# Kernel optimization log

Measured on AMD Instinct MI355X. Metric: run time of the kernel, lower is better.

Reference implementation:

```python
import jax, jax.numpy as jnp
import numpy as np

N = 100_000   # num nodes
E = 3_200_000 # num directed edges (before self-loops)
NEG_SLOPE = 0.2


def setup_inputs() -> dict:
    key = jax.random.key(0)
    ks = jax.random.split(key, 12)
    x = jax.random.normal(ks[0], (N, 2), jnp.float32)
    edge_index = jax.random.randint(ks[1], (2, E), 0, N, dtype=jnp.int32)
    # GATConv(2, 16): lin weight [2,16] (no bias), att_src/att_dst [16], out bias [16]
    W1 = jax.random.normal(ks[2], (2, 16), jnp.float32) * (1.0 / np.sqrt(2.0))
    a_src1 = jax.random.normal(ks[3], (16,), jnp.float32) * 0.25
    a_dst1 = jax.random.normal(ks[4], (16,), jnp.float32) * 0.25
    b1 = jnp.zeros((16,), jnp.float32)
    # GATConv(16, 64)
    W2 = jax.random.normal(ks[5], (16, 64), jnp.float32) * (1.0 / np.sqrt(16.0))
    a_src2 = jax.random.normal(ks[6], (64,), jnp.float32) * 0.125
    a_dst2 = jax.random.normal(ks[7], (64,), jnp.float32) * 0.125
    b2 = jnp.zeros((64,), jnp.float32)
    return {"x": x, "edge_index": edge_index,
            "W1": W1, "a_src1": a_src1, "a_dst1": a_dst1, "b1": b1,
            "W2": W2, "a_src2": a_src2, "a_dst2": a_dst2, "b2": b2}


def _gat_layer(x, src, dst, W, a_src, a_dst, b):
    # x: [N, Fin]; src/dst: [E'] (self-loops included). Single head, PyG GATConv math.
    h = x @ W                                        # [N, Fout]
    alpha_s = h @ a_src                              # [N]
    alpha_d = h @ a_dst                              # [N]
    e = jax.nn.leaky_relu(alpha_s[src] + alpha_d[dst], NEG_SLOPE)  # [E']
    # segment softmax over incoming edges of each dst node
    m = jax.ops.segment_max(e, dst, num_segments=N)
    m = jnp.where(jnp.isfinite(m), m, 0.0)           # nodes always have a self-loop, but be safe
    p = jnp.exp(e - m[dst])
    s = jax.ops.segment_sum(p, dst, num_segments=N)
    alpha = p / s[dst]                               # [E']
    out = jax.ops.segment_sum(alpha[:, None] * h[src], dst, num_segments=N)  # [N, Fout]
    return out + b


def reference(x, edge_index, W1, a_src1, a_dst1, b1, W2, a_src2, a_dst2, b2):
    # PyG GATConv adds self-loops by default
    loops = jnp.arange(N, dtype=edge_index.dtype)
    src = jnp.concatenate([edge_index[0], loops])
    dst = jnp.concatenate([edge_index[1], loops])
    h = jax.nn.relu(_gat_layer(x, src, dst, W1, a_src1, a_dst1, b1))
    h = jax.nn.relu(_gat_layer(h, src, dst, W2, a_src2, a_dst2, b2))
    return h
```

## Files before the change

kernel.cpp:

```cpp
#include <hip/hip_runtime.h>

#define NNODES 100000
#define NEDGES 3200000
#define ETOT   (NEDGES + NNODES)
#define NEG_SLOPE 0.2f
#define LOG2E 1.4426950408889634f

#define NPB 64
#define NBUCK ((NNODES + NPB - 1) / NPB)
#define NCHUNK 256
#define CHUNK_E ((ETOT + NCHUNK - 1) / NCHUNK)
#define M2 (NBUCK * NCHUNK)
#define NSB2 ((M2 + 511) / 512)

__device__ __forceinline__ unsigned short f2bf(float f) {
    unsigned u = __float_as_uint(f);
    u += 0x7FFFu + ((u >> 16) & 1u);
    return (unsigned short)(u >> 16);
}
__device__ __forceinline__ float bf2f(unsigned short h) {
    return __uint_as_float(((unsigned)h) << 16);
}

__device__ __forceinline__ void edge_sd(int e, const int* __restrict__ ei, int& s, int& d) {
    if (e < NEDGES) { s = ei[e]; d = ei[NEDGES + e]; }
    else            { s = e - NEDGES; d = s; }
}

__device__ __forceinline__ float lrelu(float v) {
    return v > 0.0f ? v : NEG_SLOPE * v;
}

__device__ __forceinline__ float edge_w(float z) {
    return __builtin_amdgcn_exp2f(lrelu(z));
}

template<int CTRL>
__device__ __forceinline__ float dpp_mov(float v) {
    return __int_as_float(__builtin_amdgcn_mov_dpp(__float_as_int(v), CTRL, 0xF, 0xF, true));
}
template<int CTRL>
__device__ __forceinline__ float dpp_add(float v) { return v + dpp_mov<CTRL>(v); }
template<int IMM>
__device__ __forceinline__ float swz(float v) {
    return __int_as_float(__builtin_amdgcn_ds_swizzle(__float_as_int(v), IMM));
}
__device__ __forceinline__ float swz16_add(float v) { return v + swz<0x401F>(v); }
__device__ __forceinline__ float row16_sum(float v) {
    v = dpp_add<0x121>(v);
    v = dpp_add<0x122>(v);
    v = dpp_add<0x124>(v);
    v = dpp_add<0x128>(v);
    return v;
}
__device__ __forceinline__ float half32_sum(float v) {
    v = row16_sum(v);
    v = swz16_add(v);
    return v;
}


__global__ void chunk_hist(const int* __restrict__ ei, int* __restrict__ H) {
    __shared__ int h[NBUCK];
    int c = blockIdx.x;
    for (int i = threadIdx.x; i < NBUCK; i += blockDim.x) h[i] = 0;
    __syncthreads();
    int lo = c * CHUNK_E, hi = lo + CHUNK_E; if (hi > ETOT) hi = ETOT;
    for (int e = lo + threadIdx.x; e < hi; e += blockDim.x) {
        int d = (e < NEDGES) ? ei[NEDGES + e] : (e - NEDGES);
        atomicAdd(&h[d >> 6], 1);
    }
    __syncthreads();
    for (int i = threadIdx.x; i < NBUCK; i += blockDim.x) H[c * NBUCK + i] = h[i];
}

__global__ void cscan_local(const int* __restrict__ H, int* __restrict__ off,
                            int* __restrict__ bsum2) {
    __shared__ int arr[512];
    int blk = blockIdx.x, t = threadIdx.x;
    int i = blk * 512 + t;
    int v = (i < M2) ? H[(i & (NCHUNK - 1)) * NBUCK + (i >> 8)] : 0;
    arr[t] = v;
    __syncthreads();
    for (int o = 1; o < 512; o <<= 1) {
        int u = (t >= o) ? arr[t - o] : 0;
        __syncthreads();
        arr[t] += u;
        __syncthreads();
    }
    if (i < M2) off[i] = arr[t] - v;
    if (t == 511) bsum2[blk] = arr[t];
}

__global__ void cscan_bsum(const int* __restrict__ bsum2, int* __restrict__ boff2) {
    __shared__ int arr[1024];
    int t = threadIdx.x;
    int v = (t < NSB2) ? bsum2[t] : 0;
    arr[t] = v;
    __syncthreads();
    for (int o = 1; o < 1024; o <<= 1) {
        int u = (t >= o) ? arr[t - o] : 0;
        __syncthreads();
        arr[t] += u;
        __syncthreads();
    }
    if (t < NSB2) boff2[t] = arr[t] - v;
}

__global__ void cscan_add(int* __restrict__ off, const int* __restrict__ boff2) {
    int i = blockIdx.x * 512 + threadIdx.x;
    if (i < M2) off[i] += boff2[blockIdx.x];
}

__global__ __launch_bounds__(1024)
void chunk_scatter(const int* __restrict__ ei, const int* __restrict__ off,
                   const int* __restrict__ H, int* __restrict__ pairs) {
    __shared__ int plds[CHUNK_E];
    __shared__ unsigned short blds[CHUNK_E];
    __shared__ int sc[2048];
    __shared__ int lcur[NBUCK];
    __shared__ int gbase[NBUCK];
    int c = blockIdx.x, t = threadIdx.x;
    for (int b = t; b < 2048; b += 1024) sc[b] = (b < NBUCK) ? H[c * NBUCK + b] : 0;
    __syncthreads();
    for (int o = 1; o < 2048; o <<= 1) {
        int i1 = t + 1024;
        int v0 = (t >= o) ? sc[t - o] : 0;
        int v1 = (i1 >= o) ? sc[i1 - o] : 0;
        __syncthreads();
        sc[t] += v0; sc[i1] += v1;
        __syncthreads();
    }
    for (int b = t; b < NBUCK; b += 1024) {
        int excl = (b == 0) ? 0 : sc[b - 1];
        lcur[b]  = excl;
        gbase[b] = off[b * NCHUNK + c] - excl;
    }
    __syncthreads();
    int lo = c * CHUNK_E, hi = lo + CHUNK_E; if (hi > ETOT) hi = ETOT;
    int n = hi - lo;
    for (int e = lo + t; e < hi; e += 1024) {
        int s, d; edge_sd(e, ei, s, d);
        int b = d >> 6;
        int slot = atomicAdd(&lcur[b], 1);
        plds[slot] = ((d & 63) << 17) | s;
        blds[slot] = (unsigned short)b;
    }
    __syncthreads();
    for (int i = t; i < n; i += 1024)
        pairs[gbase[blds[i]] + i] = plds[i];
}

__global__ void fine_sort2(const int* __restrict__ off, const int* __restrict__ pairs,
                           int* __restrict__ row_start, int* __restrict__ csr_src) {
    __shared__ int arr[NPB];
    __shared__ int cur[NPB];
    int b = blockIdx.x;
    int t = threadIdx.x;
    int base = off[b * NCHUNK];
    int bend = (b == NBUCK - 1) ? ETOT : off[(b + 1) * NCHUNK];
    if (t < NPB) arr[t] = 0;
    __syncthreads();
    for (int i = base + t; i < bend; i += blockDim.x)
        atomicAdd(&arr[pairs[i] >> 17], 1);
    __syncthreads();
    int v = (t < NPB) ? arr[t] : 0;
    __syncthreads();
    for (int o = 1; o < NPB; o <<= 1) {
        int u = (t < NPB && t >= o) ? arr[t - o] : 0;
        __syncthreads();
        if (t < NPB) arr[t] += u;
        __syncthreads();
    }
    if (t < NPB) {
        int node = b * NPB + t;
        int start = base + arr[t] - v;
        cur[t] = start;
        if (node < NNODES) row_start[node] = start;
    }
    if (b == NBUCK - 1 && t == 0) row_start[NNODES] = ETOT;
    __syncthreads();
    for (int i = base + t; i < bend; i += blockDim.x) {
        int p = pairs[i];
        int slot = atomicAdd(&cur[p >> 17], 1);
        csr_src[slot] = p & 0x1FFFF;
    }
}

__global__ void prep(const float* __restrict__ W1, const float* __restrict__ as1,
                     const float* __restrict__ ad1, const float* __restrict__ W2,
                     const float* __restrict__ as2, const float* __restrict__ ad2,
                     float* __restrict__ cvec) {
    int t = threadIdx.x;
    if (t < 2) {
        float s = 0.f, d = 0.f;
        for (int f = 0; f < 16; ++f) { s += W1[t * 16 + f] * as1[f]; d += W1[t * 16 + f] * ad1[f]; }
        cvec[t] = s * LOG2E; cvec[2 + t] = d * LOG2E;
    }
    if (t < 16) {
        float s = 0.f, d = 0.f;
        for (int f = 0; f < 64; ++f) { s += W2[t * 64 + f] * as2[f]; d += W2[t * 64 + f] * ad2[f]; }
        cvec[4 + t] = s * LOG2E; cvec[20 + t] = d * LOG2E;
    }
}

__global__ void alpha1(const float* __restrict__ x, const float* __restrict__ cvec,
                       float4* __restrict__ nrec1, float* __restrict__ ad_) {
    int n = blockIdx.x * blockDim.x + threadIdx.x;
    if (n >= NNODES) return;
    float2 xv = ((const float2*)x)[n];
    float as = xv.x * cvec[0] + xv.y * cvec[1];
    ad_[n] = xv.x * cvec[2] + xv.y * cvec[3];
    nrec1[n] = make_float4(xv.x, xv.y, as, 0.f);
}

__global__ void agg_l1(const int* __restrict__ row_start, const int* __restrict__ csr_src,
                       const float4* __restrict__ nrec1, const float* __restrict__ ad_,
                       const float* __restrict__ W1, const float* __restrict__ b1,
                       const float* __restrict__ cvec,
                       float* __restrict__ nrec2, float* __restrict__ ad2_) {
    int wave = threadIdx.x >> 6;
    int half = (threadIdx.x >> 5) & 1;
    int hlane = threadIdx.x & 31;
    int node = blockIdx.x * 8 + wave * 2 + half;
    int base = row_start[node], end = row_start[node + 1];
    float adv = ad_[node];
    float a0 = 0.f, a1 = 0.f, ss = 0.f;
    for (int i = base + hlane; i < end; i += 32) {
        int sj = csr_src[i];
        float4 r = nrec1[sj];
        float w = edge_w(r.z + adv);
        ss += w;
        a0 += w * r.x;
        a1 += w * r.y;
    }
    a0 = half32_sum(a0); a1 = half32_sum(a1); ss = half32_sum(ss);
    int f = hlane & 15;
    float v = (a0 * W1[f] + a1 * W1[16 + f]) / ss + b1[f];
    float vr = v > 0.f ? v : 0.f;
    unsigned short* grow = (unsigned short*)(nrec2 + (size_t)node * 16);
    if (hlane < 16) grow[hlane] = f2bf(vr);
    float s2 = vr * cvec[4 + f];
    float d2 = vr * cvec[20 + f];
    s2 = row16_sum(s2); d2 = row16_sum(d2);
    if (hlane == 0) {
        nrec2[(size_t)node * 16 + 8] = s2;
        ad2_[node] = d2;
    }
}

__global__ void agg_l2(const int* __restrict__ row_start, const int* __restrict__ csr_src,
                       const float* __restrict__ nrec2, const float* __restrict__ ad_,
                       const float* __restrict__ W2, const float* __restrict__ b2,
                       float* __restrict__ out) {
    __shared__ float tot[4][2][16];
    int wave = threadIdx.x >> 6;
    int half = (threadIdx.x >> 5) & 1;
    int hlane = threadIdx.x & 31;
    int node = blockIdx.x * 8 + wave * 2 + half;
    int base = row_start[node], end = row_start[node + 1];
    float adv = ad_[node];
    float acc[16];
#pragma unroll
    for (int k = 0; k < 16; ++k) acc[k] = 0.f;
    float ss = 0.f;
    for (int i = base + hlane; i < end; i += 32) {
        int sj = csr_src[i];
        const float* recf = nrec2 + (size_t)sj * 16;
        const uint4* rec4 = (const uint4*)recf;
        uint4 u0 = rec4[0], u1 = rec4[1];
        float as2v = recf[8];
        float w = edge_w(as2v + adv);
        ss += w;
        unsigned uu[8] = {u0.x, u0.y, u0.z, u0.w, u1.x, u1.y, u1.z, u1.w};
#pragma unroll
        for (int j = 0; j < 8; ++j) {
            acc[2 * j]     += w * __uint_as_float(uu[j] << 16);
            acc[2 * j + 1] += w * __uint_as_float(uu[j] & 0xFFFF0000u);
        }
    }
#pragma unroll
    for (int j = 0; j < 8; ++j) {
        float keep = (hlane & 1) ? acc[2 * j + 1] : acc[2 * j];
        float send = (hlane & 1) ? acc[2 * j]     : acc[2 * j + 1];
        acc[j] = keep + dpp_mov<0xB1>(send);
    }
#pragma unroll
    for (int j = 0; j < 4; ++j) {
        float keep = (hlane & 2) ? acc[2 * j + 1] : acc[2 * j];
        float send = (hlane & 2) ? acc[2 * j]     : acc[2 * j + 1];
        acc[j] = keep + dpp_mov<0x4E>(send);
    }
#pragma unroll
    for (int j = 0; j < 2; ++j) {
        float keep = (hlane & 4) ? acc[2 * j + 1] : acc[2 * j];
        float send = (hlane & 4) ? acc[2 * j]     : acc[2 * j + 1];
        acc[j] = keep + swz<0x101F>(send);
    }
    float r;
    {
        float keep = (hlane & 8) ? acc[1] : acc[0];
        float send = (hlane & 8) ? acc[0] : acc[1];
        r = keep + swz<0x201F>(send);
    }
    r = swz16_add(r);
    float st = half32_sum(ss);
    if (hlane < 16) tot[wave][half][hlane] = r;
    float o0 = 0.f, o1 = 0.f;
#pragma unroll
    for (int k = 0; k < 16; ++k) {
        float t = tot[wave][half][k];
        o0 += t * W2[k * 64 + hlane];
        o1 += t * W2[k * 64 + 32 + hlane];
    }
    float inv = 1.0f / st;
    o0 = o0 * inv + b2[hlane];
    o1 = o1 * inv + b2[32 + hlane];
    out[(size_t)node * 64 + hlane]      = o0 > 0.f ? o0 : 0.f;
    out[(size_t)node * 64 + 32 + hlane] = o1 > 0.f ? o1 : 0.f;
}

extern "C" void kernel_launch(void* const* d_in, const int* in_sizes, int n_in,
                              void* d_out, int out_size, void* d_ws, size_t ws_size,
                              hipStream_t stream) {
    const float* x     = (const float*)d_in[0];
    const int*   ei    = (const int*)  d_in[1];
    const float* W1    = (const float*)d_in[2];
    const float* as1w  = (const float*)d_in[3];
    const float* ad1w  = (const float*)d_in[4];
    const float* b1    = (const float*)d_in[5];
    const float* W2    = (const float*)d_in[6];
    const float* as2w  = (const float*)d_in[7];
    const float* ad2w  = (const float*)d_in[8];
    const float* b2    = (const float*)d_in[9];
    float* out = (float*)d_out;

    int* row_start = (int*)d_ws;
    int* csr_src   = row_start + (NNODES + 4);
    float* nrec2   = (float*)(csr_src + ETOT);
    float* adb     = nrec2 + (size_t)NNODES * 16;
    float* ad2b    = adb + NNODES;
    float* cvec    = ad2b + NNODES;
    int* pairs     = (int*)(cvec + 64);
    int* H         = pairs + ETOT;
    int* off       = H + M2;
    int* bsum2     = off + M2;
    int* boff2     = bsum2 + 1024;
    float4* nrec1  = (float4*)(boff2 + 1024);

    const int B = 256;
    const int NB = (NNODES + B - 1) / B;

    chunk_hist<<<NCHUNK, 1024, 0, stream>>>(ei, H);
    cscan_local<<<NSB2, 512, 0, stream>>>(H, off, bsum2);
    cscan_bsum<<<1, 1024, 0, stream>>>(bsum2, boff2);
    cscan_add<<<NSB2, 512, 0, stream>>>(off, boff2);
    chunk_scatter<<<NCHUNK, 1024, 0, stream>>>(ei, off, H, pairs);
    fine_sort2<<<NBUCK, B, 0, stream>>>(off, pairs, row_start, csr_src);

    prep<<<1, 64, 0, stream>>>(W1, as1w, ad1w, W2, as2w, ad2w, cvec);

    alpha1<<<NB, B, 0, stream>>>(x, cvec, nrec1, adb);
    agg_l1<<<NNODES / 8, B, 0, stream>>>(row_start, csr_src, nrec1, adb, W1, b1,
                                         cvec, nrec2, ad2b);

    agg_l2<<<NNODES / 8, B, 0, stream>>>(row_start, csr_src, nrec2, ad2b, W2, b2, out);
}
```

Before: 221.1 us.

## Fold scan block offsets into consumers and stage bucket pairs in LDS

Removes the cscan_add kernel by having chunk_scatter and fine_sort2 add the block-level scan offset (boff2[b>>1], valid since each 512-entry scan block covers two buckets of 256 chunks) when they read off. fine_sort2 now uses 512 threads and caches each bucket's pairs in shared memory when they fit in 4096 entries, so the second pass reads LDS instead of global memory. This saves one launch, one pass over the offset array and one global reread of pairs, at the cost of 16KB of LDS per block, which may lower occupancy.

```diff
diff --git a/kernel.cpp b/kernel.cpp
--- a/kernel.cpp
+++ b/kernel.cpp
@@ -12,6 +12,7 @@
 #define CHUNK_E ((ETOT + NCHUNK - 1) / NCHUNK)
 #define M2 (NBUCK * NCHUNK)
 #define NSB2 ((M2 + 511) / 512)
+#define FS_CAP 4096
 
 __device__ __forceinline__ unsigned short f2bf(float f) {
     unsigned u = __float_as_uint(f);
@@ -107,14 +108,10 @@
     if (t < NSB2) boff2[t] = arr[t] - v;
 }
 
-__global__ void cscan_add(int* __restrict__ off, const int* __restrict__ boff2) {
-    int i = blockIdx.x * 512 + threadIdx.x;
-    if (i < M2) off[i] += boff2[blockIdx.x];
-}
-
 __global__ __launch_bounds__(1024)
 void chunk_scatter(const int* __restrict__ ei, const int* __restrict__ off,
-                   const int* __restrict__ H, int* __restrict__ pairs) {
+                   const int* __restrict__ boff2, const int* __restrict__ H,
+                   int* __restrict__ pairs) {
     __shared__ int plds[CHUNK_E];
     __shared__ unsigned short blds[CHUNK_E];
     __shared__ int sc[2048];
@@ -134,7 +131,7 @@
     for (int b = t; b < NBUCK; b += 1024) {
         int excl = (b == 0) ? 0 : sc[b - 1];
         lcur[b]  = excl;
-        gbase[b] = off[b * NCHUNK + c] - excl;
+        gbase[b] = off[b * NCHUNK + c] + boff2[b >> 1] - excl;
     }
     __syncthreads();
     int lo = c * CHUNK_E, hi = lo + CHUNK_E; if (hi > ETOT) hi = ETOT;
@@ -151,18 +148,31 @@
         pairs[gbase[blds[i]] + i] = plds[i];
 }
 
-__global__ void fine_sort2(const int* __restrict__ off, const int* __restrict__ pairs,
-                           int* __restrict__ row_start, int* __restrict__ csr_src) {
+__global__ __launch_bounds__(512)
+void fine_sort2(const int* __restrict__ off, const int* __restrict__ boff2,
+                const int* __restrict__ pairs,
+                int* __restrict__ row_start, int* __restrict__ csr_src) {
+    __shared__ int sp[FS_CAP];
     __shared__ int arr[NPB];
     __shared__ int cur[NPB];
     int b = blockIdx.x;
     int t = threadIdx.x;
-    int base = off[b * NCHUNK];
-    int bend = (b == NBUCK - 1) ? ETOT : off[(b + 1) * NCHUNK];
+    int base = off[b * NCHUNK] + boff2[b >> 1];
+    int bend = (b == NBUCK - 1) ? ETOT : off[(b + 1) * NCHUNK] + boff2[(b + 1) >> 1];
+    int n = bend - base;
     if (t < NPB) arr[t] = 0;
     __syncthreads();
-    for (int i = base + t; i < bend; i += blockDim.x)
-        atomicAdd(&arr[pairs[i] >> 17], 1);
+    bool fits = (n <= FS_CAP);
+    if (fits) {
+        for (int i = t; i < n; i += 512) {
+            int p = pairs[base + i];
+            sp[i] = p;
+            atomicAdd(&arr[p >> 17], 1);
+        }
+    } else {
+        for (int i = t; i < n; i += 512)
+            atomicAdd(&arr[pairs[base + i] >> 17], 1);
+    }
     __syncthreads();
     int v = (t < NPB) ? arr[t] : 0;
     __syncthreads();
@@ -180,10 +190,18 @@
     }
     if (b == NBUCK - 1 && t == 0) row_start[NNODES] = ETOT;
     __syncthreads();
-    for (int i = base + t; i < bend; i += blockDim.x) {
-        int p = pairs[i];
-        int slot = atomicAdd(&cur[p >> 17], 1);
-        csr_src[slot] = p & 0x1FFFF;
+    if (fits) {
+        for (int i = t; i < n; i += 512) {
+            int p = sp[i];
+            int slot = atomicAdd(&cur[p >> 17], 1);
+            csr_src[slot] = p & 0x1FFFF;
+        }
+    } else {
+        for (int i = t; i < n; i += 512) {
+            int p = pairs[base + i];
+            int slot = atomicAdd(&cur[p >> 17], 1);
+            csr_src[slot] = p & 0x1FFFF;
+        }
     }
 }
 
@@ -354,9 +372,8 @@
     chunk_hist<<<NCHUNK, 1024, 0, stream>>>(ei, H);
     cscan_local<<<NSB2, 512, 0, stream>>>(H, off, bsum2);
     cscan_bsum<<<1, 1024, 0, stream>>>(bsum2, boff2);
-    cscan_add<<<NSB2, 512, 0, stream>>>(off, boff2);
-    chunk_scatter<<<NCHUNK, 1024, 0, stream>>>(ei, off, H, pairs);
-    fine_sort2<<<NBUCK, B, 0, stream>>>(off, pairs, row_start, csr_src);
+    chunk_scatter<<<NCHUNK, 1024, 0, stream>>>(ei, off, boff2, H, pairs);
+    fine_sort2<<<NBUCK, 512, 0, stream>>>(off, boff2, pairs, row_start, csr_src);
 
     prep<<<1, 64, 0, stream>>>(W1, as1w, ad1w, W2, as2w, ad2w, cvec);
 
```

After: 215.9 us. 1.02x faster.
